# Performance work log

Measured on AMD Instinct MI355X. Metric: run time of the kernel, lower is better.

The kernel has to match this reference:

```python
import jax, jax.numpy as jnp
import numpy as np


def setup_inputs() -> dict:
    key = jax.random.key(0)
    ks = jax.random.split(key, 7)
    D, H, M = 1024, 8, 2048
    return {
        "Q": jax.random.normal(ks[0], (1, D), dtype=jnp.float32),
        "K": jax.random.normal(ks[1], (M, D), dtype=jnp.float32),
        "V": jax.random.normal(ks[2], (M, 128, 128, 3), dtype=jnp.float32),
        "WQ": jax.random.normal(ks[3], (H, D, D), dtype=jnp.float32) * 0.02,
        "bQ": jax.random.normal(ks[4], (H, D), dtype=jnp.float32) * 0.02,
        "WK": jax.random.normal(ks[5], (H, D, D), dtype=jnp.float32) * 0.02,
        "bK": jax.random.normal(ks[6], (H, D), dtype=jnp.float32) * 0.02,
    }


def reference(Q, K, V, WQ, bQ, WK, bK):
    # Per-head linear projections (torch Linear: x @ W.T + b; W is [out, in])
    # q: [H, 1, D], k: [H, M, D]
    q = jnp.einsum("nd,hed->hne", Q, WQ) + bQ[:, None, :]
    k = jnp.einsum("md,hed->hme", K, WK) + bK[:, None, :]
    dim = K.shape[1]
    # logits: [H, 1, M]; NOTE: original divides by dim (not sqrt(dim))
    logits = jnp.einsum("hne,hme->hnm", q, k) / dim
    weights = jax.nn.softmax(logits, axis=-1)[:, 0, :]  # [H, M]
    # weighted sum over neighbor images: [H, Himg, Wimg, 3]
    out = jnp.einsum("hm,mabc->habc", weights, V)
    return out
```

## Files before the change

### kernel.cpp

```cpp
#include <hip/hip_runtime.h>

#define D     1024
#define H     8
#define M     2048
#define IMG   49152
#define IMG4  12288
#define NC    16

typedef float nfloat4 __attribute__((ext_vector_type(4)));

#define WS_Q      0
#define WS_P      8192
#define WS_BK     16384
#define WS_LOGITS 16448
#define WS_W      32832
#define WS_PART   65536

__global__ __launch_bounds__(256) void qproj_kernel(
    const float* __restrict__ Q, const float* __restrict__ WQ,
    const float* __restrict__ bQ, float* __restrict__ q_out) {
  int wave = (blockIdx.x * 256 + threadIdx.x) >> 6;
  int lane = threadIdx.x & 63;
  int h = wave >> 10;
  int e = wave & 1023;
  const float4* Wrow = (const float4*)(WQ + (size_t)(h * D + e) * D);
  const float4* Q4 = (const float4*)Q;
  float acc = 0.f;
#pragma unroll
  for (int i = 0; i < 4; ++i) {
    float4 w = Wrow[lane + i * 64];
    float4 qv = Q4[lane + i * 64];
    acc += w.x * qv.x + w.y * qv.y + w.z * qv.z + w.w * qv.w;
  }
#pragma unroll
  for (int off = 32; off; off >>= 1) acc += __shfl_xor(acc, off, 64);
  if (lane == 0) q_out[h * D + e] = acc + bQ[h * D + e];
}

__global__ __launch_bounds__(256) void pproj_kernel(
    const float* __restrict__ q, const float* __restrict__ WK,
    float* __restrict__ p) {
  int h = blockIdx.y;
  int e0 = blockIdx.x * 16;
  __shared__ float qc[16];
  if (threadIdx.x < 16) qc[threadIdx.x] = q[h * D + e0 + threadIdx.x];
  __syncthreads();
  const float4* W4 = (const float4*)(WK + (size_t)h * D * D);
  float4 acc = {0.f, 0.f, 0.f, 0.f};
#pragma unroll 4
  for (int ee = 0; ee < 16; ++ee) {
    float4 w = W4[(size_t)(e0 + ee) * (D / 4) + threadIdx.x];
    float qe = qc[ee];
    acc.x += qe * w.x;
    acc.y += qe * w.y;
    acc.z += qe * w.z;
    acc.w += qe * w.w;
  }
  float* pd = p + h * D + threadIdx.x * 4;
  atomicAdd(pd + 0, acc.x);
  atomicAdd(pd + 1, acc.y);
  atomicAdd(pd + 2, acc.z);
  atomicAdd(pd + 3, acc.w);
}

__global__ __launch_bounds__(512) void bkdot_kernel(
    const float* __restrict__ q, const float* __restrict__ bK,
    float* __restrict__ bkdot) {
  int h = threadIdx.x >> 6;
  int lane = threadIdx.x & 63;
  const float4* q4 = (const float4*)(q + h * D);
  const float4* b4 = (const float4*)(bK + h * D);
  float acc = 0.f;
#pragma unroll
  for (int i = 0; i < 4; ++i) {
    float4 a = q4[lane + i * 64];
    float4 b = b4[lane + i * 64];
    acc += a.x * b.x + a.y * b.y + a.z * b.z + a.w * b.w;
  }
#pragma unroll
  for (int off = 32; off; off >>= 1) acc += __shfl_xor(acc, off, 64);
  if (lane == 0) bkdot[h] = acc;
}

__global__ __launch_bounds__(256) void logits_kernel(
    const float* __restrict__ K, const float* __restrict__ p,
    const float* __restrict__ bkdot, float* __restrict__ logits) {
  int wave = (blockIdx.x * 256 + threadIdx.x) >> 6;
  int lane = threadIdx.x & 63;
  int m = wave;
  const float4* K4 = (const float4*)(K + (size_t)m * D);
  float acc[H];
#pragma unroll
  for (int h = 0; h < H; ++h) acc[h] = 0.f;
#pragma unroll
  for (int i = 0; i < 4; ++i) {
    float4 kv = K4[lane + i * 64];
#pragma unroll
    for (int h = 0; h < H; ++h) {
      float4 pv = ((const float4*)(p + h * D))[lane + i * 64];
      acc[h] += kv.x * pv.x + kv.y * pv.y + kv.z * pv.z + kv.w * pv.w;
    }
  }
#pragma unroll
  for (int h = 0; h < H; ++h) {
    float a = acc[h];
#pragma unroll
    for (int off = 32; off; off >>= 1) a += __shfl_xor(a, off, 64);
    if (lane == 0) logits[h * M + m] = (a + bkdot[h]) * (1.0f / (float)D);
  }
}

__global__ __launch_bounds__(256) void softmax_kernel(
    const float* __restrict__ logits, float* __restrict__ w) {
  int h = blockIdx.x;
  int lane = threadIdx.x & 63;
  int wid = threadIdx.x >> 6;
  __shared__ float sred[8];
  float l[8];
  float mx = -1e30f;
#pragma unroll
  for (int i = 0; i < 8; ++i) {
    l[i] = logits[h * M + threadIdx.x + i * 256];
    mx = fmaxf(mx, l[i]);
  }
#pragma unroll
  for (int off = 32; off; off >>= 1) mx = fmaxf(mx, __shfl_xor(mx, off, 64));
  if (lane == 0) sred[wid] = mx;
  __syncthreads();
  float bmax = fmaxf(fmaxf(sred[0], sred[1]), fmaxf(sred[2], sred[3]));
  float ev[8];
  float s = 0.f;
#pragma unroll
  for (int i = 0; i < 8; ++i) {
    ev[i] = __expf(l[i] - bmax);
    s += ev[i];
  }
#pragma unroll
  for (int off = 32; off; off >>= 1) s += __shfl_xor(s, off, 64);
  if (lane == 0) sred[4 + wid] = s;
  __syncthreads();
  float tot = sred[4] + sred[5] + sred[6] + sred[7];
  float inv = 1.0f / tot;
#pragma unroll
  for (int i = 0; i < 8; ++i)
    w[h * M + threadIdx.x + i * 256] = ev[i] * inv;
}

__global__ __launch_bounds__(256) void out_partial_kernel(
    const float* __restrict__ V, const float* __restrict__ w,
    float* __restrict__ part) {
  int mc = blockIdx.y;
  int m0 = mc * 128;
  int c4 = blockIdx.x * 256 + threadIdx.x;
  __shared__ float wc[H][128];
  for (int i = threadIdx.x; i < H * 128; i += 256)
    wc[i >> 7][i & 127] = w[(i >> 7) * M + m0 + (i & 127)];
  __syncthreads();
  const nfloat4* V4 = (const nfloat4*)V;
  float4 acc[H];
#pragma unroll
  for (int h = 0; h < H; ++h) acc[h] = make_float4(0.f, 0.f, 0.f, 0.f);
  for (int mm = 0; mm < 128; mm += 8) {
    nfloat4 v[8];
#pragma unroll
    for (int j = 0; j < 8; ++j)
      v[j] = __builtin_nontemporal_load(&V4[(size_t)(m0 + mm + j) * IMG4 + c4]);
#pragma unroll
    for (int h = 0; h < H; ++h) {
#pragma unroll
      for (int j = 0; j < 8; ++j) {
        float wj = wc[h][mm + j];
        acc[h].x += wj * v[j].x;
        acc[h].y += wj * v[j].y;
        acc[h].z += wj * v[j].z;
        acc[h].w += wj * v[j].w;
      }
    }
  }
  nfloat4* P4 = (nfloat4*)part;
#pragma unroll
  for (int h = 0; h < H; ++h) {
    nfloat4 o = {acc[h].x, acc[h].y, acc[h].z, acc[h].w};
    __builtin_nontemporal_store(o, &P4[((size_t)mc * H + h) * IMG4 + c4]);
  }
}

__global__ __launch_bounds__(256) void out_reduce_kernel(
    const float* __restrict__ part, float* __restrict__ out) {
  int idx = blockIdx.x * 256 + threadIdx.x;
  const nfloat4* P4 = (const nfloat4*)part;
  float4 s = make_float4(0.f, 0.f, 0.f, 0.f);
#pragma unroll
  for (int mc = 0; mc < NC; ++mc) {
    nfloat4 v = __builtin_nontemporal_load(&P4[(size_t)mc * (H * IMG4) + idx]);
    s.x += v.x; s.y += v.y; s.z += v.z; s.w += v.w;
  }
  nfloat4 o = {s.x, s.y, s.z, s.w};
  __builtin_nontemporal_store(o, &((nfloat4*)out)[idx]);
}

extern "C" void kernel_launch(void* const* d_in, const int* in_sizes, int n_in,
                              void* d_out, int out_size, void* d_ws, size_t ws_size,
                              hipStream_t stream) {
  const float* Q  = (const float*)d_in[0];
  const float* K  = (const float*)d_in[1];
  const float* V  = (const float*)d_in[2];
  const float* WQ = (const float*)d_in[3];
  const float* bQ = (const float*)d_in[4];
  const float* WK = (const float*)d_in[5];
  const float* bK = (const float*)d_in[6];
  float* out = (float*)d_out;
  float* ws = (float*)d_ws;

  float* q_ws     = ws + WS_Q;
  float* p_ws     = ws + WS_P;
  float* bk_ws    = ws + WS_BK;
  float* log_ws   = ws + WS_LOGITS;
  float* w_ws     = ws + WS_W;
  float* part_ws  = ws + WS_PART;

  (void)hipMemsetAsync(p_ws, 0, (size_t)H * D * sizeof(float), stream);

  qproj_kernel<<<dim3(2048), dim3(256), 0, stream>>>(Q, WQ, bQ, q_ws);
  pproj_kernel<<<dim3(64, H), dim3(256), 0, stream>>>(q_ws, WK, p_ws);
  bkdot_kernel<<<dim3(1), dim3(512), 0, stream>>>(q_ws, bK, bk_ws);
  logits_kernel<<<dim3(512), dim3(256), 0, stream>>>(K, p_ws, bk_ws, log_ws);
  softmax_kernel<<<dim3(H), dim3(256), 0, stream>>>(log_ws, w_ws);
  out_partial_kernel<<<dim3(48, NC), dim3(256), 0, stream>>>(V, w_ws, part_ws);
  out_reduce_kernel<<<dim3(384), dim3(256), 0, stream>>>(part_ws, out);
}
```

Before: 584.5 us.

## Drop bias-dot kernel, fold memset into qproj, and split work finer

Removes the bkdot kernel and its term from the logits. q·bK is a constant per head, and softmax is invariant to a per-row shift, so the result is unchanged. Replaces the hipMemsetAsync with zeroing inside qproj's first block. Halves the per-block work in pproj and in out_partial: NC goes from 16 to 32, so twice as many blocks stream V. The cost is doubled partial-buffer traffic and twice as many reduction terms. The in-kernel zeroing relies on qproj finishing before pproj's atomics on the same stream, which stream order guarantees.

```diff
diff --git a/kernel.cpp b/kernel.cpp
--- a/kernel.cpp
+++ b/kernel.cpp
@@ -5,20 +5,25 @@
 #define M     2048
 #define IMG   49152
 #define IMG4  12288
-#define NC    16
+#define NC    32
 
 typedef float nfloat4 __attribute__((ext_vector_type(4)));
 
 #define WS_Q      0
 #define WS_P      8192
-#define WS_BK     16384
 #define WS_LOGITS 16448
 #define WS_W      32832
 #define WS_PART   65536
 
 __global__ __launch_bounds__(256) void qproj_kernel(
     const float* __restrict__ Q, const float* __restrict__ WQ,
-    const float* __restrict__ bQ, float* __restrict__ q_out) {
+    const float* __restrict__ bQ, float* __restrict__ q_out,
+    float* __restrict__ p_zero) {
+  if (blockIdx.x == 0) {
+#pragma unroll
+    for (int i = 0; i < (H * D) / 256; ++i)
+      p_zero[i * 256 + threadIdx.x] = 0.f;
+  }
   int wave = (blockIdx.x * 256 + threadIdx.x) >> 6;
   int lane = threadIdx.x & 63;
   int h = wave >> 10;
@@ -41,14 +46,14 @@
     const float* __restrict__ q, const float* __restrict__ WK,
     float* __restrict__ p) {
   int h = blockIdx.y;
-  int e0 = blockIdx.x * 16;
-  __shared__ float qc[16];
-  if (threadIdx.x < 16) qc[threadIdx.x] = q[h * D + e0 + threadIdx.x];
+  int e0 = blockIdx.x * 8;
+  __shared__ float qc[8];
+  if (threadIdx.x < 8) qc[threadIdx.x] = q[h * D + e0 + threadIdx.x];
   __syncthreads();
   const float4* W4 = (const float4*)(WK + (size_t)h * D * D);
   float4 acc = {0.f, 0.f, 0.f, 0.f};
-#pragma unroll 4
-  for (int ee = 0; ee < 16; ++ee) {
+#pragma unroll
+  for (int ee = 0; ee < 8; ++ee) {
     float4 w = W4[(size_t)(e0 + ee) * (D / 4) + threadIdx.x];
     float qe = qc[ee];
     acc.x += qe * w.x;
@@ -63,28 +68,9 @@
   atomicAdd(pd + 3, acc.w);
 }
 
-__global__ __launch_bounds__(512) void bkdot_kernel(
-    const float* __restrict__ q, const float* __restrict__ bK,
-    float* __restrict__ bkdot) {
-  int h = threadIdx.x >> 6;
-  int lane = threadIdx.x & 63;
-  const float4* q4 = (const float4*)(q + h * D);
-  const float4* b4 = (const float4*)(bK + h * D);
-  float acc = 0.f;
-#pragma unroll
-  for (int i = 0; i < 4; ++i) {
-    float4 a = q4[lane + i * 64];
-    float4 b = b4[lane + i * 64];
-    acc += a.x * b.x + a.y * b.y + a.z * b.z + a.w * b.w;
-  }
-#pragma unroll
-  for (int off = 32; off; off >>= 1) acc += __shfl_xor(acc, off, 64);
-  if (lane == 0) bkdot[h] = acc;
-}
-
 __global__ __launch_bounds__(256) void logits_kernel(
     const float* __restrict__ K, const float* __restrict__ p,
-    const float* __restrict__ bkdot, float* __restrict__ logits) {
+    float* __restrict__ logits) {
   int wave = (blockIdx.x * 256 + threadIdx.x) >> 6;
   int lane = threadIdx.x & 63;
   int m = wave;
@@ -106,7 +92,7 @@
     float a = acc[h];
 #pragma unroll
     for (int off = 32; off; off >>= 1) a += __shfl_xor(a, off, 64);
-    if (lane == 0) logits[h * M + m] = (a + bkdot[h]) * (1.0f / (float)D);
+    if (lane == 0) logits[h * M + m] = a * (1.0f / (float)D);
   }
 }
 
@@ -150,17 +136,17 @@
     const float* __restrict__ V, const float* __restrict__ w,
     float* __restrict__ part) {
   int mc = blockIdx.y;
-  int m0 = mc * 128;
+  int m0 = mc * 64;
   int c4 = blockIdx.x * 256 + threadIdx.x;
-  __shared__ float wc[H][128];
-  for (int i = threadIdx.x; i < H * 128; i += 256)
-    wc[i >> 7][i & 127] = w[(i >> 7) * M + m0 + (i & 127)];
+  __shared__ float wc[H][64];
+  for (int i = threadIdx.x; i < H * 64; i += 256)
+    wc[i >> 6][i & 63] = w[(i >> 6) * M + m0 + (i & 63)];
   __syncthreads();
   const nfloat4* V4 = (const nfloat4*)V;
   float4 acc[H];
 #pragma unroll
   for (int h = 0; h < H; ++h) acc[h] = make_float4(0.f, 0.f, 0.f, 0.f);
-  for (int mm = 0; mm < 128; mm += 8) {
+  for (int mm = 0; mm < 64; mm += 8) {
     nfloat4 v[8];
 #pragma unroll
     for (int j = 0; j < 8; ++j)
@@ -208,23 +194,18 @@
   const float* WQ = (const float*)d_in[3];
   const float* bQ = (const float*)d_in[4];
   const float* WK = (const float*)d_in[5];
-  const float* bK = (const float*)d_in[6];
   float* out = (float*)d_out;
   float* ws = (float*)d_ws;
 
   float* q_ws     = ws + WS_Q;
   float* p_ws     = ws + WS_P;
-  float* bk_ws    = ws + WS_BK;
   float* log_ws   = ws + WS_LOGITS;
   float* w_ws     = ws + WS_W;
   float* part_ws  = ws + WS_PART;
 
-  (void)hipMemsetAsync(p_ws, 0, (size_t)H * D * sizeof(float), stream);
-
-  qproj_kernel<<<dim3(2048), dim3(256), 0, stream>>>(Q, WQ, bQ, q_ws);
-  pproj_kernel<<<dim3(64, H), dim3(256), 0, stream>>>(q_ws, WK, p_ws);
-  bkdot_kernel<<<dim3(1), dim3(512), 0, stream>>>(q_ws, bK, bk_ws);
-  logits_kernel<<<dim3(512), dim3(256), 0, stream>>>(K, p_ws, bk_ws, log_ws);
+  qproj_kernel<<<dim3(2048), dim3(256), 0, stream>>>(Q, WQ, bQ, q_ws, p_ws);
+  pproj_kernel<<<dim3(128, H), dim3(256), 0, stream>>>(q_ws, WK, p_ws);
+  logits_kernel<<<dim3(512), dim3(256), 0, stream>>>(K, p_ws, log_ws);
   softmax_kernel<<<dim3(H), dim3(256), 0, stream>>>(log_ws, w_ws);
   out_partial_kernel<<<dim3(48, NC), dim3(256), 0, stream>>>(V, w_ws, part_ws);
   out_reduce_kernel<<<dim3(384), dim3(256), 0, stream>>>(part_ws, out);
```

New measurement: 607.9 us. +4.0%, slower.
